# Kernel optimization log

Measured on AMD Instinct MI355X. Metric: run time of the kernel, lower is better.

The kernel has to match this reference:

```python
import jax, jax.numpy as jnp
import numpy as np

N_NODES = 50000
N_EDGES = 800000
D = 128
H = 8
HD = D // H
N_NTYPES = 3
N_ETYPES = 5
LN_EPS = 1e-5


def setup_inputs() -> dict:
    key = jax.random.key(0)
    ks = jax.random.split(key, 16)
    inp = {
        "x": jax.random.normal(ks[0], (N_NODES, D), dtype=jnp.float32),
        "edge_index": jax.random.randint(ks[1], (2, N_EDGES), 0, N_NODES),
        "edge_type": jax.random.randint(ks[2], (N_EDGES,), 0, N_ETYPES),
        "node_type": jax.random.randint(ks[3], (N_NODES,), 0, N_NTYPES),
        # per-(node_type, head) QKV projections, per-(edge_type, head) K transform
        "W_Q": jax.random.normal(ks[4], (N_NTYPES, H, HD, HD), dtype=jnp.float32) * 0.02,
        "W_K": jax.random.normal(ks[5], (N_NTYPES, H, HD, HD), dtype=jnp.float32) * 0.02,
        "W_V": jax.random.normal(ks[6], (N_NTYPES, H, HD, HD), dtype=jnp.float32) * 0.02,
        "W_edge": jax.random.normal(ks[7], (N_ETYPES, H, HD, HD), dtype=jnp.float32) * 0.02,
        "mu": jnp.ones((H, N_ETYPES), dtype=jnp.float32),
        "W_out": jax.random.normal(ks[8], (D, D), dtype=jnp.float32) * 0.02,
        "b_out": jnp.zeros((D,), dtype=jnp.float32),
        "ln1_g": jnp.ones((D,), dtype=jnp.float32),
        "ln1_b": jnp.zeros((D,), dtype=jnp.float32),
        "W1": jax.random.normal(ks[9], (D, 4 * D), dtype=jnp.float32) * 0.02,
        "b1": jnp.zeros((4 * D,), dtype=jnp.float32),
        "W2": jax.random.normal(ks[10], (4 * D, D), dtype=jnp.float32) * 0.02,
        "b2": jnp.zeros((D,), dtype=jnp.float32),
        "ln2_g": jnp.ones((D,), dtype=jnp.float32),
        "ln2_b": jnp.zeros((D,), dtype=jnp.float32),
    }
    return inp


def _layer_norm(y, g, b):
    m = y.mean(-1, keepdims=True)
    v = ((y - m) ** 2).mean(-1, keepdims=True)
    return (y - m) * jax.lax.rsqrt(v + LN_EPS) * g + b


def reference(x, edge_index, edge_type, node_type,
              W_Q, W_K, W_V, W_edge, mu,
              W_out, b_out, ln1_g, ln1_b, W1, b1, W2, b2, ln2_g, ln2_b):
    N = x.shape[0]
    xh = x.reshape(N, H, HD)  # heads vectorized (concat of per-head slices)

    # type-specific QKV: small fixed loop over node types, masked select
    Q = jnp.zeros_like(xh)
    K = jnp.zeros_like(xh)
    V = jnp.zeros_like(xh)
    for t in range(N_NTYPES):
        m = (node_type == t)[:, None, None]
        Q = jnp.where(m, jnp.einsum('nhd,hdf->nhf', xh, W_Q[t]), Q)
        K = jnp.where(m, jnp.einsum('nhd,hdf->nhf', xh, W_K[t]), K)
        V = jnp.where(m, jnp.einsum('nhd,hdf->nhf', xh, W_V[t]), V)

    src, dst = edge_index[0], edge_index[1]
    q_dst = Q[dst]   # [E,H,HD]
    k_src = K[src]   # [E,H,HD]

    # edge-type-specific K transform
    kt = jnp.zeros_like(k_src)
    for et in range(N_ETYPES):
        m = (edge_type == et)[:, None, None]
        kt = jnp.where(m, jnp.einsum('ehd,hdf->ehf', k_src, W_edge[et]), kt)

    scores = (q_dst * kt).sum(-1) / jnp.sqrt(jnp.float32(HD))  # [E,H]
    scores = scores * mu[:, edge_type].T                       # mu per edge type, per head

    # sparse softmax over incoming edges of each dst node, per head
    smax = jax.ops.segment_max(scores, dst, num_segments=N)
    ex = jnp.exp(scores - smax[dst])
    den = jax.ops.segment_sum(ex, dst, num_segments=N)
    w = ex / (den[dst] + 1e-10)                                 # [E,H]

    agg = jax.ops.segment_sum(V[src] * w[..., None], dst, num_segments=N)  # [N,H,HD]
    mh = agg.reshape(N, D) @ W_out + b_out  # dropout is identity in eval

    h = _layer_norm(x + mh, ln1_g, ln1_b)
    ffn = jax.nn.gelu(h @ W1 + b1, approximate=False) @ W2 + b2
    return _layer_norm(h + ffn, ln2_g, ln2_b)
```

## Files before the change

### kernel.cpp

```cpp
#include <hip/hip_runtime.h>
#include <hip/hip_bf16.h>

#define N_NODESC 50000
#define N_EDGESC 800000
#define DD 128
#define HH 8
#define HDIM 16
#define N_NT 3
#define N_ET 5
#define NPB 196
#define NEB 400
#define NFB 512

#define KV8_OFF    ((size_t)0)
#define QT8_OFF    ((size_t)12800000)
#define XP_OFF     ((size_t)44800000)
#define T_OFF      ((size_t)0)
#define AGG_OFF    ((size_t)57600000)
#define H1B_OFF    ((size_t)70400000)
#define WOUTT_OFF  ((size_t)83200000)
#define W1T_OFF    ((size_t)83232768)
#define W2T_OFF    ((size_t)83363840)
#define WALL_OFF   ((size_t)83494912)
#define EDATA_OFF  ((size_t)84183040)
#define ROWS_OFF   ((size_t)87383040)
#define ORIG_OFF   ((size_t)87583104)
#define DEG_OFF    ((size_t)87783104)
#define TOFS_OFF   ((size_t)87983104)
#define BH_OFF     ((size_t)87983168)
#define BB_OFF     ((size_t)87985536)
#define TMP_OFF    ((size_t)87988928)
#define RLOC_OFF   ((size_t)91188928)
#define CSUM_OFF   ((size_t)91389056)

using short8 = __attribute__((ext_vector_type(8))) short;
using f32x4  = __attribute__((ext_vector_type(4))) float;
using f32x2  = __attribute__((ext_vector_type(2))) float;

__device__ __forceinline__ ushort f2b(float f) {
    __hip_bfloat16 h = __float2bfloat16(f);
    return *(ushort*)&h;
}
__device__ __forceinline__ float b2f(ushort u) {
    __hip_bfloat16 h = *(__hip_bfloat16*)&u;
    return __bfloat162float(h);
}
__device__ __forceinline__ f32x2 pk0(unsigned int w) {
    return __builtin_amdgcn_cvt_pk_f32_fp8((int)w, false);
}
__device__ __forceinline__ f32x2 pk1(unsigned int w) {
    return __builtin_amdgcn_cvt_pk_f32_fp8((int)w, true);
}

__global__ __launch_bounds__(256) void prep_a(
    const float* __restrict__ Wout, const float* __restrict__ W1, const float* __restrict__ W2,
    const float* __restrict__ WQ, const float* __restrict__ Wk, const float* __restrict__ Wv,
    const float* __restrict__ We, const float* __restrict__ mu,
    ushort* __restrict__ Woutt, ushort* __restrict__ W1t, ushort* __restrict__ W2t,
    ushort* __restrict__ Wall,
    const int* __restrict__ ntype, int* __restrict__ bh,
    const int* __restrict__ dst, int* __restrict__ deg, unsigned int* __restrict__ tmp)
{
    const int b = blockIdx.x, tid = threadIdx.x;
    if (b < 1920) {
        const int gid = b * 256 + tid;
        if (gid < 16384) {
            const int nn = gid >> 7, k = gid & 127;
            Woutt[gid] = f2b(Wout[k * 128 + nn]);
        } else if (gid < 81920) {
            const int i = gid - 16384;
            const int nn = i >> 7, k = i & 127;
            W1t[i] = f2b(W1[k * 512 + nn]);
        } else if (gid < 147456) {
            const int i = gid - 81920;
            const int nn = i >> 9, k = i & 511;
            W2t[i] = f2b(W2[k * 128 + nn]);
        } else {
            const int idx = gid - 147456;
            const int t = idx / (896 * 128);
            const int rem = idx % (896 * 128);
            const int c = rem / 128, k = rem % 128;
            const int hk = k >> 4, ck = k & 15;
            float v = 0.f;
            if (c < 128) {
                const int hc = c >> 4, j = c & 15;
                if (hk == hc) v = 4.f * Wk[((t * HH + hc) * HDIM + ck) * HDIM + j];
            } else if (c < 256) {
                const int c2 = c - 128, hc = c2 >> 4, j = c2 & 15;
                if (hk == hc) v = 4.f * Wv[((t * HH + hc) * HDIM + ck) * HDIM + j];
            } else {
                const int cq = c - 256, et = cq >> 7, dd = cq & 127;
                const int hq = dd >> 4, j = dd & 15;
                if (hk == hq) {
                    const float* wq = WQ + ((t * HH + hq) * HDIM + ck) * HDIM;
                    const float* we = We + ((et * HH + hq) * HDIM + j) * HDIM;
                    float s = 0.f;
#pragma unroll
                    for (int f = 0; f < 16; f++) s = fmaf(wq[f], we[f], s);
                    v = 64.f * mu[hq * N_ET + et] * s;
                }
            }
            Wall[idx] = f2b(v);
        }
    } else if (b < 1920 + NPB) {
        const int bc = b - 1920;
        const int wave = tid >> 6, lane = tid & 63;
        const int n = bc * 256 + tid;
        const int t = (n < N_NODESC) ? ntype[n] : -1;
        const unsigned long long m0 = __ballot(t == 0);
        const unsigned long long m1 = __ballot(t == 1);
        const unsigned long long m2 = __ballot(t == 2);
        __shared__ int wcnt[4][3];
        if (lane == 0) {
            wcnt[wave][0] = (int)__popcll(m0);
            wcnt[wave][1] = (int)__popcll(m1);
            wcnt[wave][2] = (int)__popcll(m2);
        }
        __syncthreads();
        if (tid < 3)
            bh[tid * NPB + bc] = wcnt[0][tid] + wcnt[1][tid] + wcnt[2][tid] + wcnt[3][tid];
    } else {
        for (int e = (b - 1920 - NPB) * 256 + tid; e < N_EDGESC; e += NEB * 256) {
            const int nd = dst[e];
            const unsigned int p = (unsigned int)atomicAdd(&deg[nd], 1);
            tmp[e] = (p << 16) | (unsigned int)nd;
        }
    }
}

__global__ __launch_bounds__(256) void prep_b(
    const int* __restrict__ bh, const int* __restrict__ deg,
    int* __restrict__ bb, int* __restrict__ tofs,
    int* __restrict__ rloc, int* __restrict__ csum)
{
    __shared__ int part[256];
    const int tid = threadIdx.x;
    if (blockIdx.x == 0) {
        const int base3 = tid * 3;
        int e0 = (base3 + 0 < 588) ? bh[base3 + 0] : 0;
        int e1 = (base3 + 1 < 588) ? bh[base3 + 1] : 0;
        int e2 = (base3 + 2 < 588) ? bh[base3 + 2] : 0;
        const int l0 = e0, l1 = e0 + e1, l2 = l1 + e2;
        part[tid] = l2;
        __syncthreads();
        for (int off = 1; off < 256; off <<= 1) {
            const int u = (tid >= off) ? part[tid - off] : 0;
            __syncthreads();
            part[tid] += u;
            __syncthreads();
        }
        const int tb = part[tid] - l2;
        if (base3 + 0 < 588) bb[base3 + 0] = tb;
        if (base3 + 1 < 588) bb[base3 + 1] = tb + l0;
        if (base3 + 2 < 588) bb[base3 + 2] = tb + l1;
        __syncthreads();
        if (tid == 0) {
            tofs[0] = 0;
            tofs[1] = bb[NPB];
            tofs[2] = bb[2 * NPB];
            tofs[3] = N_NODESC;
        }
    } else {
        const int c = blockIdx.x - 1;
        const int n = c * 256 + tid;
        const int vdeg = (n < N_NODESC) ? deg[n] : 0;
        part[tid] = vdeg;
        __syncthreads();
        for (int off = 1; off < 256; off <<= 1) {
            const int u = (tid >= off) ? part[tid - off] : 0;
            __syncthreads();
            part[tid] += u;
            __syncthreads();
        }
        if (n <= N_NODESC) rloc[n] = part[tid] - vdeg;
        if (tid == 255) csum[c] = part[255];
    }
}

__global__ __launch_bounds__(256) void prep_c(
    const int* __restrict__ ntype, const float* __restrict__ x,
    const int* __restrict__ src, const int* __restrict__ etype,
    const int* __restrict__ bb, const int* __restrict__ rloc, const int* __restrict__ csum,
    const unsigned int* __restrict__ tmp,
    int* __restrict__ origof, ushort* __restrict__ Xp, int* __restrict__ rows,
    int* __restrict__ edata)
{
    const int b = blockIdx.x, tid = threadIdx.x;
    __shared__ int cb[256];
    {
        const int v = (tid < NPB) ? csum[tid] : 0;
        cb[tid] = v;
        __syncthreads();
        for (int off = 1; off < 256; off <<= 1) {
            const int u = (tid >= off) ? cb[tid - off] : 0;
            __syncthreads();
            cb[tid] += u;
            __syncthreads();
        }
        const int incl = cb[tid];
        __syncthreads();
        cb[tid] = incl - v;
        __syncthreads();
    }

    if (b < NPB) {
        const int wave = tid >> 6, lane = tid & 63;
        const int n = b * 256 + tid;
        const int t = (n < N_NODESC) ? ntype[n] : -1;
        const unsigned long long m0 = __ballot(t == 0);
        const unsigned long long m1 = __ballot(t == 1);
        const unsigned long long m2 = __ballot(t == 2);
        __shared__ int wcnt[4][3];
        __shared__ int sp[256];
        if (lane == 0) {
            wcnt[wave][0] = (int)__popcll(m0);
            wcnt[wave][1] = (int)__popcll(m1);
            wcnt[wave][2] = (int)__popcll(m2);
        }
        __syncthreads();
        int p = -1;
        if (n < N_NODESC) {
            int basew = 0;
#pragma unroll
            for (int w = 0; w < 4; w++) if (w < wave) basew += wcnt[w][t];
            const unsigned long long mt = (t == 0) ? m0 : (t == 1) ? m1 : m2;
            const unsigned long long mlt = ((unsigned long long)1 << lane) - 1;
            p = bb[t * NPB + b] + basew + (int)__popcll(mt & mlt);
            origof[p] = n;
        }
        if (n <= N_NODESC) rows[n] = cb[b] + rloc[n];
        sp[tid] = p;
        __syncthreads();
        for (int i = tid; i < 256 * 16; i += 256) {
            const int nn = i >> 4, c = (i & 15) << 3;
            const int pp = sp[nn];
            if (pp < 0) continue;
            const int n2 = b * 256 + nn;
            const float4 v0 = *(const float4*)(x + (size_t)n2 * DD + c);
            const float4 v1 = *(const float4*)(x + (size_t)n2 * DD + c + 4);
            ushort o[8] = {f2b(v0.x), f2b(v0.y), f2b(v0.z), f2b(v0.w),
                           f2b(v1.x), f2b(v1.y), f2b(v1.z), f2b(v1.w)};
            *(uint4*)(Xp + (size_t)pp * DD + c) = *(uint4*)o;
        }
    } else {
        for (int e = (b - NPB) * 256 + tid; e < N_EDGESC; e += NFB * 256) {
            const unsigned int v = tmp[e];
            const int nd = (int)(v & 0xffffu);
            const int p = (int)(v >> 16);
            edata[cb[nd >> 8] + rloc[nd] + p] = src[e] | (etype[e] << 16);
        }
    }
}

#define LDP 40

__global__ __launch_bounds__(256) void proj_gemm(
    const ushort* __restrict__ Xp, const ushort* __restrict__ Wall,
    const int* __restrict__ tofs, const int* __restrict__ origof,
    ushort* __restrict__ KV8, unsigned char* __restrict__ Qt8)
{
    const int t = blockIdx.z;
    const int rs = tofs[t], re = tofs[t + 1];
    const int mBase = rs + blockIdx.x * 128;
    if (mBase >= re) return;
    const int nBase = blockIdx.y * 128;
    const ushort* Bt = Wall + (size_t)t * 896 * 128;

    __shared__ ushort As[128 * LDP];
    __shared__ ushort Bs[128 * LDP];
    const int tid = threadIdx.x;
    const int lane = tid & 63, wave = tid >> 6;
    const int mw = (wave >> 1) * 64, nw = (wave & 1) * 64;
    const int l15 = lane & 15, q8 = (lane >> 4) * 8;

    f32x4 acc[4][4];
#pragma unroll
    for (int i = 0; i < 4; i++)
#pragma unroll
        for (int j = 0; j < 4; j++) acc[i][j] = (f32x4){0.f, 0.f, 0.f, 0.f};

    const int r0 = tid >> 2, c0 = (tid & 3) * 8;
    int rA0 = mBase + r0;      if (rA0 >= N_NODESC) rA0 = N_NODESC - 1;
    int rA1 = mBase + r0 + 64; if (rA1 >= N_NODESC) rA1 = N_NODESC - 1;

    for (int kk = 0; kk < 128; kk += 32) {
        short8 a0 = *(const short8*)(Xp + (size_t)rA0 * DD + kk + c0);
        short8 a1 = *(const short8*)(Xp + (size_t)rA1 * DD + kk + c0);
        short8 b0 = *(const short8*)(Bt + (size_t)(nBase + r0) * 128 + kk + c0);
        short8 b1 = *(const short8*)(Bt + (size_t)(nBase + r0 + 64) * 128 + kk + c0);
        *(short8*)&As[r0 * LDP + c0] = a0;
        *(short8*)&As[(r0 + 64) * LDP + c0] = a1;
        *(short8*)&Bs[r0 * LDP + c0] = b0;
        *(short8*)&Bs[(r0 + 64) * LDP + c0] = b1;
        __syncthreads();
        short8 af[4], bf[4];
#pragma unroll
        for (int i = 0; i < 4; i++)
            af[i] = *(const short8*)&As[(mw + i * 16 + l15) * LDP + q8];
#pragma unroll
        for (int j = 0; j < 4; j++)
            bf[j] = *(const short8*)&Bs[(nw + j * 16 + l15) * LDP + q8];
#pragma unroll
        for (int i = 0; i < 4; i++)
#pragma unroll
            for (int j = 0; j < 4; j++)
                acc[i][j] = __builtin_amdgcn_mfma_f32_16x16x32_bf16(af[i], bf[j], acc[i][j], 0, 0, 0);
        __syncthreads();
    }

    unsigned char* kvb = (unsigned char*)KV8;
    const int rq = (lane >> 4) * 4;
#pragma unroll
    for (int i = 0; i < 4; i++) {
#pragma unroll
        for (int r = 0; r < 4; r++) {
            const int gm = mBase + mw + i * 16 + rq + r;
            if (gm >= re) continue;
            const int og = origof[gm];
#pragma unroll
            for (int j = 0; j < 4; j++) {
                const int gn = nBase + nw + j * 16 + l15;
                const float v = acc[i][j][r];
                const unsigned char b8 =
                    (unsigned char)(__builtin_amdgcn_cvt_pk_fp8_f32(v, v, 0, false) & 0xff);
                if (gn < 256) kvb[(size_t)og * 256 + gn] = b8;
                else          Qt8[(size_t)og * 640 + (gn - 256)] = b8;
            }
        }
    }
}

__global__ __launch_bounds__(128) void edgeagg_kernel(
    const int* __restrict__ rowstart, const int* __restrict__ edata,
    const unsigned char* __restrict__ Qt8, const unsigned char* __restrict__ KV8,
    ushort* __restrict__ agg)
{
    const int w = threadIdx.x >> 6;
    const int lane = threadIdx.x & 63;
    const int n = blockIdx.x * 2 + w;
    const int slot = lane >> 3;
    const int h = lane & 7;

    __shared__ uint4 qs8s[2][40];
    if (lane < 40)
        qs8s[w][lane] = ((const uint4*)(Qt8 + (size_t)n * 640))[lane];
    __syncthreads();
    const uint* qbase = (const uint*)&qs8s[w][0];

    const int s0 = rowstart[n], s1 = rowstart[n + 1];
    const float qsc = 1.44269504f / 1024.f;

    float acc[16];
#pragma unroll
    for (int j = 0; j < 16; j++) acc[j] = 0.f;
    float den = 0.f;

    for (int i = s0 + slot; i < s1; i += 8) {
        const int ed = edata[i];
        const int sn = ed & 0xffff;
        const int et = ed >> 16;
        const unsigned char* kvp = KV8 + ((size_t)sn << 8);
        const uint4 kw = *(const uint4*)(kvp + (h << 4));
        const uint4 vw = *(const uint4*)(kvp + 128 + (h << 4));
        const uint4 qw = *(const uint4*)(qbase + (et << 5) + (h << 2));

        const f32x2 q0 = pk0(qw.x), q1 = pk1(qw.x), q2 = pk0(qw.y), q3 = pk1(qw.y);
        const f32x2 q4 = pk0(qw.z), q5 = pk1(qw.z), q6 = pk0(qw.w), q7 = pk1(qw.w);
        const f32x2 k0 = pk0(kw.x), k1 = pk1(kw.x), k2 = pk0(kw.y), k3 = pk1(kw.y);
        const f32x2 k4 = pk0(kw.z), k5 = pk1(kw.z), k6 = pk0(kw.w), k7 = pk1(kw.w);

        float pa = q0.x * k0.x;
        float pb = q0.y * k0.y;
        float pc = q1.x * k1.x;
        float pd = q1.y * k1.y;
        pa = fmaf(q2.x, k2.x, pa); pb = fmaf(q2.y, k2.y, pb);
        pc = fmaf(q3.x, k3.x, pc); pd = fmaf(q3.y, k3.y, pd);
        pa = fmaf(q4.x, k4.x, pa); pb = fmaf(q4.y, k4.y, pb);
        pc = fmaf(q5.x, k5.x, pc); pd = fmaf(q5.y, k5.y, pd);
        pa = fmaf(q6.x, k6.x, pa); pb = fmaf(q6.y, k6.y, pb);
        pc = fmaf(q7.x, k7.x, pc); pd = fmaf(q7.y, k7.y, pd);

        const float ex = exp2f(((pa + pb) + (pc + pd)) * qsc);
        den += ex;

        const f32x2 v0 = pk0(vw.x), v1 = pk1(vw.x), v2 = pk0(vw.y), v3 = pk1(vw.y);
        const f32x2 v4 = pk0(vw.z), v5 = pk1(vw.z), v6 = pk0(vw.w), v7 = pk1(vw.w);
        acc[0]  = fmaf(ex, v0.x, acc[0]);  acc[1]  = fmaf(ex, v0.y, acc[1]);
        acc[2]  = fmaf(ex, v1.x, acc[2]);  acc[3]  = fmaf(ex, v1.y, acc[3]);
        acc[4]  = fmaf(ex, v2.x, acc[4]);  acc[5]  = fmaf(ex, v2.y, acc[5]);
        acc[6]  = fmaf(ex, v3.x, acc[6]);  acc[7]  = fmaf(ex, v3.y, acc[7]);
        acc[8]  = fmaf(ex, v4.x, acc[8]);  acc[9]  = fmaf(ex, v4.y, acc[9]);
        acc[10] = fmaf(ex, v5.x, acc[10]); acc[11] = fmaf(ex, v5.y, acc[11]);
        acc[12] = fmaf(ex, v6.x, acc[12]); acc[13] = fmaf(ex, v6.y, acc[13]);
        acc[14] = fmaf(ex, v7.x, acc[14]); acc[15] = fmaf(ex, v7.y, acc[15]);
    }

    {
        const int b0 = slot & 1, b1 = slot & 2, b2 = slot & 4;
#pragma unroll
        for (int j = 0; j < 8; j++) {
            const float v = b0 ? acc[j] : acc[j + 8];
            const float r = __shfl_xor(v, 8);
            acc[j] = (b0 ? acc[j + 8] : acc[j]) + r;
        }
#pragma unroll
        for (int j = 0; j < 4; j++) {
            const float v = b1 ? acc[j] : acc[j + 4];
            const float r = __shfl_xor(v, 16);
            acc[j] = (b1 ? acc[j + 4] : acc[j]) + r;
        }
#pragma unroll
        for (int j = 0; j < 2; j++) {
            const float v = b2 ? acc[j] : acc[j + 2];
            const float r = __shfl_xor(v, 32);
            acc[j] = (b2 ? acc[j + 2] : acc[j]) + r;
        }
        den += __shfl_xor(den, 8);
        den += __shfl_xor(den, 16);
        den += __shfl_xor(den, 32);
    }
    const float rr = 0.25f / (den + 1e-10f);
    const int fb = (h << 4) + ((slot & 1) << 3) + ((slot & 2) << 1) + ((slot & 4) >> 1);
    ushort o2[2] = { f2b(acc[0] * rr), f2b(acc[1] * rr) };
    *(uint*)&agg[((size_t)n << 7) + fb] = *(uint*)o2;
}

template<int KT, int EPI>
__global__ __launch_bounds__(256) void mfma_gemm(
    const ushort* __restrict__ A, const ushort* __restrict__ Bt,
    const float* __restrict__ bias,
    const float* __restrict__ residF, const ushort* __restrict__ residB,
    const float* __restrict__ g, const float* __restrict__ b,
    float* __restrict__ outF, ushort* __restrict__ outB, int ldOut)
{
    __shared__ ushort As[128 * LDP];
    __shared__ ushort Bs[128 * LDP];
    __shared__ float red[2][2][128];
    const int tid = threadIdx.x;
    const int lane = tid & 63, wave = tid >> 6;
    const int mw = (wave >> 1) * 64, nw = (wave & 1) * 64;
    const int mBase = blockIdx.x * 128, nBase = blockIdx.y * 128;
    const int l15 = lane & 15, q8 = (lane >> 4) * 8;

    f32x4 acc[4][4];
#pragma unroll
    for (int i = 0; i < 4; i++)
#pragma unroll
        for (int j = 0; j < 4; j++) acc[i][j] = (f32x4){0.f, 0.f, 0.f, 0.f};

    const int r0 = tid >> 2;
    const int c0 = (tid & 3) * 8;

    for (int kk = 0; kk < KT; kk += 32) {
        const ushort* pa = A  + (size_t)(mBase + r0) * KT + kk + c0;
        const ushort* pb = Bt + (size_t)(nBase + r0) * KT + kk + c0;
        short8 a0 = *(const short8*)pa;
        short8 a1 = *(const short8*)(pa + (size_t)64 * KT);
        short8 b0 = *(const short8*)pb;
        short8 b1 = *(const short8*)(pb + (size_t)64 * KT);
        *(short8*)&As[r0 * LDP + c0] = a0;
        *(short8*)&As[(r0 + 64) * LDP + c0] = a1;
        *(short8*)&Bs[r0 * LDP + c0] = b0;
        *(short8*)&Bs[(r0 + 64) * LDP + c0] = b1;
        __syncthreads();

        short8 af[4], bf[4];
#pragma unroll
        for (int i = 0; i < 4; i++)
            af[i] = *(const short8*)&As[(mw + i * 16 + l15) * LDP + q8];
#pragma unroll
        for (int j = 0; j < 4; j++)
            bf[j] = *(const short8*)&Bs[(nw + j * 16 + l15) * LDP + q8];
#pragma unroll
        for (int i = 0; i < 4; i++)
#pragma unroll
            for (int j = 0; j < 4; j++)
                acc[i][j] = __builtin_amdgcn_mfma_f32_16x16x32_bf16(af[i], bf[j], acc[i][j], 0, 0, 0);
        __syncthreads();
    }

    const int rq = (lane >> 4) * 4;

    if (EPI == 0) {
#pragma unroll
        for (int i = 0; i < 4; i++) {
#pragma unroll
            for (int r = 0; r < 4; r++) {
                const int gm = mBase + mw + i * 16 + rq + r;
                if (gm >= N_NODESC) continue;
#pragma unroll
                for (int j = 0; j < 4; j++) {
                    const int gn = nBase + nw + j * 16 + l15;
                    float v = acc[i][j][r] + bias[gn];
                    v = 0.5f * v * (1.f + erff(v * 0.70710678118654752f));
                    outB[(size_t)gm * ldOut + gn] = f2b(v);
                }
            }
        }
    } else {
        float biasv[4], gv[4], bv[4];
#pragma unroll
        for (int j = 0; j < 4; j++) {
            const int gn = nw + j * 16 + l15;
            biasv[j] = bias[gn]; gv[j] = g[gn]; bv[j] = b[gn];
        }
#pragma unroll
        for (int i = 0; i < 4; i++) {
#pragma unroll
            for (int r = 0; r < 4; r++) {
                const int row = mw + i * 16 + rq + r;
                const int gm = mBase + row;
                float s = 0.f, ss = 0.f;
#pragma unroll
                for (int j = 0; j < 4; j++) {
                    const int gn = nw + j * 16 + l15;
                    float v = acc[i][j][r] + biasv[j];
                    if (EPI == 1) v += (gm < N_NODESC) ? residF[(size_t)gm * DD + gn] : 0.f;
                    else          v += (gm < N_NODESC) ? b2f(residB[(size_t)gm * DD + gn]) : 0.f;
                    acc[i][j][r] = v;
                    s += v; ss += v * v;
                }
                s  += __shfl_xor(s, 1);  s  += __shfl_xor(s, 2);  s  += __shfl_xor(s, 4);  s  += __shfl_xor(s, 8);
                ss += __shfl_xor(ss, 1); ss += __shfl_xor(ss, 2); ss += __shfl_xor(ss, 4); ss += __shfl_xor(ss, 8);
                if (l15 == 0) { red[0][nw >> 6][row] = s; red[1][nw >> 6][row] = ss; }
            }
        }
        __syncthreads();
#pragma unroll
        for (int i = 0; i < 4; i++) {
#pragma unroll
            for (int r = 0; r < 4; r++) {
                const int row = mw + i * 16 + rq + r;
                const int gm = mBase + row;
                if (gm >= N_NODESC) continue;
                const float s  = red[0][0][row] + red[0][1][row];
                const float ss = red[1][0][row] + red[1][1][row];
                const float mean = s * (1.f / 128.f);
                const float var  = ss * (1.f / 128.f) - mean * mean;
                const float rstd = rsqrtf(var + 1e-5f);
#pragma unroll
                for (int j = 0; j < 4; j++) {
                    const int gn = nw + j * 16 + l15;
                    const float o = (acc[i][j][r] - mean) * rstd * gv[j] + bv[j];
                    if (EPI == 1) outB[(size_t)gm * DD + gn] = f2b(o);
                    else          outF[(size_t)gm * DD + gn] = o;
                }
            }
        }
    }
}

extern "C" void kernel_launch(void* const* d_in, const int* in_sizes, int n_in,
                              void* d_out, int out_size, void* d_ws, size_t ws_size,
                              hipStream_t stream)
{
    const float* x     = (const float*)d_in[0];
    const int*   ei    = (const int*)d_in[1];
    const int*   etyp  = (const int*)d_in[2];
    const int*   ntype = (const int*)d_in[3];
    const float* Wq    = (const float*)d_in[4];
    const float* Wk    = (const float*)d_in[5];
    const float* Wv    = (const float*)d_in[6];
    const float* We    = (const float*)d_in[7];
    const float* mu    = (const float*)d_in[8];
    const float* Wout  = (const float*)d_in[9];
    const float* bout  = (const float*)d_in[10];
    const float* g1    = (const float*)d_in[11];
    const float* b1ln  = (const float*)d_in[12];
    const float* W1    = (const float*)d_in[13];
    const float* b1    = (const float*)d_in[14];
    const float* W2    = (const float*)d_in[15];
    const float* b2    = (const float*)d_in[16];
    const float* g2    = (const float*)d_in[17];
    const float* b2ln  = (const float*)d_in[18];
    float* out = (float*)d_out;

    char* ws = (char*)d_ws;
    ushort*        KV8   = (ushort*)(ws + KV8_OFF);
    unsigned char* Qt8   = (unsigned char*)(ws + QT8_OFF);
    ushort*        Xp    = (ushort*)(ws + XP_OFF);
    ushort*        T     = (ushort*)(ws + T_OFF);
    ushort*        agg   = (ushort*)(ws + AGG_OFF);
    ushort*        h1b   = (ushort*)(ws + H1B_OFF);
    ushort*        Woutt = (ushort*)(ws + WOUTT_OFF);
    ushort*        W1t   = (ushort*)(ws + W1T_OFF);
    ushort*        W2t   = (ushort*)(ws + W2T_OFF);
    ushort*        Wall  = (ushort*)(ws + WALL_OFF);
    int*           edata = (int*)(ws + EDATA_OFF);
    int*           rows  = (int*)(ws + ROWS_OFF);
    int*           origof= (int*)(ws + ORIG_OFF);
    int*           deg   = (int*)(ws + DEG_OFF);
    int*           tofs  = (int*)(ws + TOFS_OFF);
    int*           bh    = (int*)(ws + BH_OFF);
    int*           bb    = (int*)(ws + BB_OFF);
    unsigned int*  tmp   = (unsigned int*)(ws + TMP_OFF);
    int*           rloc  = (int*)(ws + RLOC_OFF);
    int*           csum  = (int*)(ws + CSUM_OFF);

    const int* srcA = ei;
    const int* dstA = ei + N_EDGESC;

    (void)hipMemsetAsync(ws + DEG_OFF, 0, 200000, stream);

    prep_a<<<1920 + NPB + NEB, 256, 0, stream>>>(
        Wout, W1, W2, Wq, Wk, Wv, We, mu, Woutt, W1t, W2t, Wall,
        ntype, bh, dstA, deg, tmp);
    prep_b<<<1 + NPB, 256, 0, stream>>>(bh, deg, bb, tofs, rloc, csum);
    prep_c<<<NPB + NFB, 256, 0, stream>>>(ntype, x, srcA, etyp, bb, rloc, csum, tmp,
                                          origof, Xp, rows, edata);

    proj_gemm<<<dim3(394, 7, 3), 256, 0, stream>>>(Xp, Wall, tofs, origof, KV8, Qt8);
    edgeagg_kernel<<<N_NODESC / 2, 128, 0, stream>>>(rows, edata, Qt8,
                                                     (const unsigned char*)KV8, agg);

    mfma_gemm<128, 1><<<391, 256, 0, stream>>>(agg, Woutt, bout, x, nullptr, g1, b1ln, nullptr, h1b, 128);
    mfma_gemm<128, 0><<<dim3(391, 4), 256, 0, stream>>>(h1b, W1t, b1, nullptr, nullptr, nullptr, nullptr, nullptr, T, 512);
    mfma_gemm<512, 2><<<391, 256, 0, stream>>>(T, W2t, b2, nullptr, h1b, g2, b2ln, out, nullptr, 128);
}
```

Before: 356.3 us.

## Fuse output projection, LayerNorms and FFN into one tail kernel

Replaces the three separate MFMA GEMM launches (out-proj+LN1, W1+GELU, W2+LN2) with a single kernel on 64-row tiles. The LN1 output stays in shared memory, and the 512-wide hidden activation is produced and consumed in 128-column chunks without touching global memory. This removes the round trips of h1b and the large T intermediate through HBM plus two launches. In exchange it uses smaller M tiles with more syncs and weight reloads per block, and it also changes the LDS padding LDP from 40 to 36, which affects proj_gemm too.

```diff
diff --git a/kernel.cpp b/kernel.cpp
--- a/kernel.cpp
+++ b/kernel.cpp
@@ -15,9 +15,7 @@
 #define KV8_OFF    ((size_t)0)
 #define QT8_OFF    ((size_t)12800000)
 #define XP_OFF     ((size_t)44800000)
-#define T_OFF      ((size_t)0)
 #define AGG_OFF    ((size_t)57600000)
-#define H1B_OFF    ((size_t)70400000)
 #define WOUTT_OFF  ((size_t)83200000)
 #define W1T_OFF    ((size_t)83232768)
 #define W2T_OFF    ((size_t)83363840)
@@ -50,6 +48,9 @@
 }
 __device__ __forceinline__ f32x2 pk1(unsigned int w) {
     return __builtin_amdgcn_cvt_pk_f32_fp8((int)w, true);
+}
+__device__ __forceinline__ float gelu_f(float v) {
+    return 0.5f * v * (1.f + erff(v * 0.70710678118654752f));
 }
 
 __global__ __launch_bounds__(256) void prep_a(
@@ -252,7 +253,7 @@
     }
 }
 
-#define LDP 40
+#define LDP 36
 
 __global__ __launch_bounds__(256) void proj_gemm(
     const ushort* __restrict__ Xp, const ushort* __restrict__ Wall,
@@ -425,112 +426,210 @@
     *(uint*)&agg[((size_t)n << 7) + fb] = *(uint*)o2;
 }
 
-template<int KT, int EPI>
-__global__ __launch_bounds__(256) void mfma_gemm(
-    const ushort* __restrict__ A, const ushort* __restrict__ Bt,
-    const float* __restrict__ bias,
-    const float* __restrict__ residF, const ushort* __restrict__ residB,
-    const float* __restrict__ g, const float* __restrict__ b,
-    float* __restrict__ outF, ushort* __restrict__ outB, int ldOut)
+#define LDH 132
+
+__global__ __launch_bounds__(256) void fused_tail(
+    const ushort* __restrict__ agg, const ushort* __restrict__ Woutt,
+    const ushort* __restrict__ W1t, const ushort* __restrict__ W2t,
+    const float* __restrict__ x,
+    const float* __restrict__ bout, const float* __restrict__ g1, const float* __restrict__ b1ln,
+    const float* __restrict__ b1, const float* __restrict__ b2,
+    const float* __restrict__ g2, const float* __restrict__ b2ln,
+    float* __restrict__ out)
 {
-    __shared__ ushort As[128 * LDP];
+    __shared__ ushort Hs[64 * LDH];
+    __shared__ ushort As[64 * LDP];
     __shared__ ushort Bs[128 * LDP];
-    __shared__ float red[2][2][128];
+    __shared__ float red[2][2][64];
+
     const int tid = threadIdx.x;
     const int lane = tid & 63, wave = tid >> 6;
-    const int mw = (wave >> 1) * 64, nw = (wave & 1) * 64;
-    const int mBase = blockIdx.x * 128, nBase = blockIdx.y * 128;
-    const int l15 = lane & 15, q8 = (lane >> 4) * 8;
-
-    f32x4 acc[4][4];
-#pragma unroll
-    for (int i = 0; i < 4; i++)
-#pragma unroll
-        for (int j = 0; j < 4; j++) acc[i][j] = (f32x4){0.f, 0.f, 0.f, 0.f};
-
-    const int r0 = tid >> 2;
-    const int c0 = (tid & 3) * 8;
-
-    for (int kk = 0; kk < KT; kk += 32) {
-        const ushort* pa = A  + (size_t)(mBase + r0) * KT + kk + c0;
-        const ushort* pb = Bt + (size_t)(nBase + r0) * KT + kk + c0;
-        short8 a0 = *(const short8*)pa;
-        short8 a1 = *(const short8*)(pa + (size_t)64 * KT);
-        short8 b0 = *(const short8*)pb;
-        short8 b1 = *(const short8*)(pb + (size_t)64 * KT);
-        *(short8*)&As[r0 * LDP + c0] = a0;
-        *(short8*)&As[(r0 + 64) * LDP + c0] = a1;
-        *(short8*)&Bs[r0 * LDP + c0] = b0;
-        *(short8*)&Bs[(r0 + 64) * LDP + c0] = b1;
-        __syncthreads();
-
-        short8 af[4], bf[4];
-#pragma unroll
-        for (int i = 0; i < 4; i++)
-            af[i] = *(const short8*)&As[(mw + i * 16 + l15) * LDP + q8];
+    const int wm = wave >> 1, wn = wave & 1;
+    const int l15 = lane & 15, q8 = (lane >> 4) * 8, rq = (lane >> 4) * 4;
+    const int mBase = blockIdx.x * 64;
+
+    const int rA = tid >> 2, c0 = (tid & 3) * 8;
+    int rowA = mBase + rA; if (rowA >= N_NODESC) rowA = N_NODESC - 1;
+
+    f32x4 acc1[2][4], acc2[2][4];
+#pragma unroll
+    for (int i = 0; i < 2; i++)
+#pragma unroll
+        for (int j = 0; j < 4; j++) {
+            acc1[i][j] = (f32x4){0.f, 0.f, 0.f, 0.f};
+            acc2[i][j] = (f32x4){0.f, 0.f, 0.f, 0.f};
+        }
+
+    for (int kk = 0; kk < 128; kk += 32) {
+        short8 a0 = *(const short8*)(agg + (size_t)rowA * DD + kk + c0);
+        short8 b0 = *(const short8*)(Woutt + (size_t)rA * 128 + kk + c0);
+        short8 b1r = *(const short8*)(Woutt + (size_t)(rA + 64) * 128 + kk + c0);
+        *(short8*)&As[rA * LDP + c0] = a0;
+        *(short8*)&Bs[rA * LDP + c0] = b0;
+        *(short8*)&Bs[(rA + 64) * LDP + c0] = b1r;
+        __syncthreads();
+        short8 af[2], bf[4];
+#pragma unroll
+        for (int i = 0; i < 2; i++)
+            af[i] = *(const short8*)&As[(wm * 32 + i * 16 + l15) * LDP + q8];
 #pragma unroll
         for (int j = 0; j < 4; j++)
-            bf[j] = *(const short8*)&Bs[(nw + j * 16 + l15) * LDP + q8];
-#pragma unroll
-        for (int i = 0; i < 4; i++)
+            bf[j] = *(const short8*)&Bs[(wn * 64 + j * 16 + l15) * LDP + q8];
+#pragma unroll
+        for (int i = 0; i < 2; i++)
 #pragma unroll
             for (int j = 0; j < 4; j++)
-                acc[i][j] = __builtin_amdgcn_mfma_f32_16x16x32_bf16(af[i], bf[j], acc[i][j], 0, 0, 0);
-        __syncthreads();
-    }
-
-    const int rq = (lane >> 4) * 4;
-
-    if (EPI == 0) {
-#pragma unroll
-        for (int i = 0; i < 4; i++) {
+                acc1[i][j] = __builtin_amdgcn_mfma_f32_16x16x32_bf16(af[i], bf[j], acc1[i][j], 0, 0, 0);
+        __syncthreads();
+    }
+
+    {
+        float boutv[4], gv[4], bv[4];
+#pragma unroll
+        for (int j = 0; j < 4; j++) {
+            const int gn = wn * 64 + j * 16 + l15;
+            boutv[j] = bout[gn]; gv[j] = g1[gn]; bv[j] = b1ln[gn];
+        }
+#pragma unroll
+        for (int i = 0; i < 2; i++) {
 #pragma unroll
             for (int r = 0; r < 4; r++) {
-                const int gm = mBase + mw + i * 16 + rq + r;
-                if (gm >= N_NODESC) continue;
-#pragma unroll
-                for (int j = 0; j < 4; j++) {
-                    const int gn = nBase + nw + j * 16 + l15;
-                    float v = acc[i][j][r] + bias[gn];
-                    v = 0.5f * v * (1.f + erff(v * 0.70710678118654752f));
-                    outB[(size_t)gm * ldOut + gn] = f2b(v);
-                }
-            }
-        }
-    } else {
-        float biasv[4], gv[4], bv[4];
-#pragma unroll
-        for (int j = 0; j < 4; j++) {
-            const int gn = nw + j * 16 + l15;
-            biasv[j] = bias[gn]; gv[j] = g[gn]; bv[j] = b[gn];
-        }
-#pragma unroll
-        for (int i = 0; i < 4; i++) {
-#pragma unroll
-            for (int r = 0; r < 4; r++) {
-                const int row = mw + i * 16 + rq + r;
+                const int row = wm * 32 + i * 16 + rq + r;
                 const int gm = mBase + row;
                 float s = 0.f, ss = 0.f;
 #pragma unroll
                 for (int j = 0; j < 4; j++) {
-                    const int gn = nw + j * 16 + l15;
-                    float v = acc[i][j][r] + biasv[j];
-                    if (EPI == 1) v += (gm < N_NODESC) ? residF[(size_t)gm * DD + gn] : 0.f;
-                    else          v += (gm < N_NODESC) ? b2f(residB[(size_t)gm * DD + gn]) : 0.f;
-                    acc[i][j][r] = v;
+                    const int gn = wn * 64 + j * 16 + l15;
+                    float v = acc1[i][j][r] + boutv[j];
+                    v += (gm < N_NODESC) ? x[(size_t)gm * DD + gn] : 0.f;
+                    acc1[i][j][r] = v;
                     s += v; ss += v * v;
                 }
                 s  += __shfl_xor(s, 1);  s  += __shfl_xor(s, 2);  s  += __shfl_xor(s, 4);  s  += __shfl_xor(s, 8);
                 ss += __shfl_xor(ss, 1); ss += __shfl_xor(ss, 2); ss += __shfl_xor(ss, 4); ss += __shfl_xor(ss, 8);
-                if (l15 == 0) { red[0][nw >> 6][row] = s; red[1][nw >> 6][row] = ss; }
+                if (l15 == 0) { red[0][wn][row] = s; red[1][wn][row] = ss; }
             }
         }
         __syncthreads();
 #pragma unroll
-        for (int i = 0; i < 4; i++) {
+        for (int i = 0; i < 2; i++) {
 #pragma unroll
             for (int r = 0; r < 4; r++) {
-                const int row = mw + i * 16 + rq + r;
+                const int row = wm * 32 + i * 16 + rq + r;
+                const float s  = red[0][0][row] + red[0][1][row];
+                const float ss = red[1][0][row] + red[1][1][row];
+                const float mean = s * (1.f / 128.f);
+                const float var  = ss * (1.f / 128.f) - mean * mean;
+                const float rstd = rsqrtf(var + 1e-5f);
+#pragma unroll
+                for (int j = 0; j < 4; j++) {
+                    const int gn = wn * 64 + j * 16 + l15;
+                    const float o = (acc1[i][j][r] - mean) * rstd * gv[j] + bv[j];
+                    Hs[row * LDH + gn] = f2b(o);
+                }
+            }
+        }
+        __syncthreads();
+    }
+
+    for (int nb = 0; nb < 4; nb++) {
+#pragma unroll
+        for (int i = 0; i < 2; i++)
+#pragma unroll
+            for (int j = 0; j < 4; j++) acc1[i][j] = (f32x4){0.f, 0.f, 0.f, 0.f};
+
+        for (int kk = 0; kk < 128; kk += 32) {
+            short8 b0 = *(const short8*)(W1t + (size_t)(nb * 128 + rA) * 128 + kk + c0);
+            short8 b1r = *(const short8*)(W1t + (size_t)(nb * 128 + rA + 64) * 128 + kk + c0);
+            *(short8*)&Bs[rA * LDP + c0] = b0;
+            *(short8*)&Bs[(rA + 64) * LDP + c0] = b1r;
+            __syncthreads();
+            short8 af[2], bf[4];
+#pragma unroll
+            for (int i = 0; i < 2; i++)
+                af[i] = *(const short8*)&Hs[(wm * 32 + i * 16 + l15) * LDH + kk + q8];
+#pragma unroll
+            for (int j = 0; j < 4; j++)
+                bf[j] = *(const short8*)&Bs[(wn * 64 + j * 16 + l15) * LDP + q8];
+#pragma unroll
+            for (int i = 0; i < 2; i++)
+#pragma unroll
+                for (int j = 0; j < 4; j++)
+                    acc1[i][j] = __builtin_amdgcn_mfma_f32_16x16x32_bf16(af[i], bf[j], acc1[i][j], 0, 0, 0);
+            __syncthreads();
+        }
+
+        float b1v[4];
+#pragma unroll
+        for (int j = 0; j < 4; j++)
+            b1v[j] = b1[nb * 128 + wn * 64 + j * 16 + l15];
+
+        for (int kk2 = 0; kk2 < 4; kk2++) {
+            short8 b0 = *(const short8*)(W2t + (size_t)rA * 512 + nb * 128 + kk2 * 32 + c0);
+            short8 b1r = *(const short8*)(W2t + (size_t)(rA + 64) * 512 + nb * 128 + kk2 * 32 + c0);
+            *(short8*)&Bs[rA * LDP + c0] = b0;
+            *(short8*)&Bs[(rA + 64) * LDP + c0] = b1r;
+            if (wn == (kk2 >> 1)) {
+                const int j0 = 2 * (kk2 & 1);
+#pragma unroll
+                for (int i = 0; i < 2; i++)
+#pragma unroll
+                    for (int jj = 0; jj < 2; jj++)
+#pragma unroll
+                        for (int r = 0; r < 4; r++) {
+                            const int row = wm * 32 + i * 16 + rq + r;
+                            const float v = gelu_f(acc1[i][j0 + jj][r] + b1v[j0 + jj]);
+                            As[row * LDP + jj * 16 + l15] = f2b(v);
+                        }
+            }
+            __syncthreads();
+            short8 af[2], bf[4];
+#pragma unroll
+            for (int i = 0; i < 2; i++)
+                af[i] = *(const short8*)&As[(wm * 32 + i * 16 + l15) * LDP + q8];
+#pragma unroll
+            for (int j = 0; j < 4; j++)
+                bf[j] = *(const short8*)&Bs[(wn * 64 + j * 16 + l15) * LDP + q8];
+#pragma unroll
+            for (int i = 0; i < 2; i++)
+#pragma unroll
+                for (int j = 0; j < 4; j++)
+                    acc2[i][j] = __builtin_amdgcn_mfma_f32_16x16x32_bf16(af[i], bf[j], acc2[i][j], 0, 0, 0);
+            __syncthreads();
+        }
+    }
+
+    {
+        float b2v[4], gv[4], bv[4];
+#pragma unroll
+        for (int j = 0; j < 4; j++) {
+            const int gn = wn * 64 + j * 16 + l15;
+            b2v[j] = b2[gn]; gv[j] = g2[gn]; bv[j] = b2ln[gn];
+        }
+#pragma unroll
+        for (int i = 0; i < 2; i++) {
+#pragma unroll
+            for (int r = 0; r < 4; r++) {
+                const int row = wm * 32 + i * 16 + rq + r;
+                float s = 0.f, ss = 0.f;
+#pragma unroll
+                for (int j = 0; j < 4; j++) {
+                    const int gn = wn * 64 + j * 16 + l15;
+                    float v = acc2[i][j][r] + b2v[j] + b2f(Hs[row * LDH + gn]);
+                    acc2[i][j][r] = v;
+                    s += v; ss += v * v;
+                }
+                s  += __shfl_xor(s, 1);  s  += __shfl_xor(s, 2);  s  += __shfl_xor(s, 4);  s  += __shfl_xor(s, 8);
+                ss += __shfl_xor(ss, 1); ss += __shfl_xor(ss, 2); ss += __shfl_xor(ss, 4); ss += __shfl_xor(ss, 8);
+                if (l15 == 0) { red[0][wn][row] = s; red[1][wn][row] = ss; }
+            }
+        }
+        __syncthreads();
+#pragma unroll
+        for (int i = 0; i < 2; i++) {
+#pragma unroll
+            for (int r = 0; r < 4; r++) {
+                const int row = wm * 32 + i * 16 + rq + r;
                 const int gm = mBase + row;
                 if (gm >= N_NODESC) continue;
                 const float s  = red[0][0][row] + red[0][1][row];
@@ -540,10 +639,8 @@
                 const float rstd = rsqrtf(var + 1e-5f);
 #pragma unroll
                 for (int j = 0; j < 4; j++) {
-                    const int gn = nw + j * 16 + l15;
-                    const float o = (acc[i][j][r] - mean) * rstd * gv[j] + bv[j];
-                    if (EPI == 1) outB[(size_t)gm * DD + gn] = f2b(o);
-                    else          outF[(size_t)gm * DD + gn] = o;
+                    const int gn = wn * 64 + j * 16 + l15;
+                    out[(size_t)gm * DD + gn] = (acc2[i][j][r] - mean) * rstd * gv[j] + bv[j];
                 }
             }
         }
@@ -579,9 +676,7 @@
     ushort*        KV8   = (ushort*)(ws + KV8_OFF);
     unsigned char* Qt8   = (unsigned char*)(ws + QT8_OFF);
     ushort*        Xp    = (ushort*)(ws + XP_OFF);
-    ushort*        T     = (ushort*)(ws + T_OFF);
     ushort*        agg   = (ushort*)(ws + AGG_OFF);
-    ushort*        h1b   = (ushort*)(ws + H1B_OFF);
     ushort*        Woutt = (ushort*)(ws + WOUTT_OFF);
     ushort*        W1t   = (ushort*)(ws + W1T_OFF);
     ushort*        W2t   = (ushort*)(ws + W2T_OFF);
@@ -613,7 +708,6 @@
     edgeagg_kernel<<<N_NODESC / 2, 128, 0, stream>>>(rows, edata, Qt8,
                                                      (const unsigned char*)KV8, agg);
 
-    mfma_gemm<128, 1><<<391, 256, 0, stream>>>(agg, Woutt, bout, x, nullptr, g1, b1ln, nullptr, h1b, 128);
-    mfma_gemm<128, 0><<<dim3(391, 4), 256, 0, stream>>>(h1b, W1t, b1, nullptr, nullptr, nullptr, nullptr, nullptr, T, 512);
-    mfma_gemm<512, 2><<<391, 256, 0, stream>>>(T, W2t, b2, nullptr, h1b, g2, b2ln, out, nullptr, 128);
-}
+    fused_tail<<<782, 256, 0, stream>>>(agg, Woutt, W1t, W2t, x,
+                                        bout, g1, b1ln, b1, b2, g2, b2ln, out);
+}
```

New measurement: 342.4 us. 3.9% less time.

## Fuse output projection, LayerNorms and FFN into one per-row-tile tail kernel

Applied to the files above, without the earlier changes.

Replaces the three separate GEMM launches (W_out+LN1, W1+GELU, W2+LN2) with one kernel. Each wave owns 16 rows and runs the full tail, keeping the h1 and GELU intermediates in shared memory instead of writing the 512-wide intermediate to global. Weight fragments are read directly from global (L2) with no shared staging, and there is no inter-wave reduction. This removes intermediate HBM traffic and launch overhead, but adds redundant weight reads and less data reuse per block. The shared-memory padding for proj_gemm also changes from 40 to 36.

```diff
diff --git a/kernel.cpp b/kernel.cpp
--- a/kernel.cpp
+++ b/kernel.cpp
@@ -15,9 +15,7 @@
 #define KV8_OFF    ((size_t)0)
 #define QT8_OFF    ((size_t)12800000)
 #define XP_OFF     ((size_t)44800000)
-#define T_OFF      ((size_t)0)
 #define AGG_OFF    ((size_t)57600000)
-#define H1B_OFF    ((size_t)70400000)
 #define WOUTT_OFF  ((size_t)83200000)
 #define W1T_OFF    ((size_t)83232768)
 #define W2T_OFF    ((size_t)83363840)
@@ -50,6 +48,9 @@
 }
 __device__ __forceinline__ f32x2 pk1(unsigned int w) {
     return __builtin_amdgcn_cvt_pk_f32_fp8((int)w, true);
+}
+__device__ __forceinline__ float gelu_f(float v) {
+    return 0.5f * v * (1.f + erff(v * 0.70710678118654752f));
 }
 
 __global__ __launch_bounds__(256) void prep_a(
@@ -252,7 +253,7 @@
     }
 }
 
-#define LDP 40
+#define LDP 36
 
 __global__ __launch_bounds__(256) void proj_gemm(
     const ushort* __restrict__ Xp, const ushort* __restrict__ Wall,
@@ -425,126 +426,128 @@
     *(uint*)&agg[((size_t)n << 7) + fb] = *(uint*)o2;
 }
 
-template<int KT, int EPI>
-__global__ __launch_bounds__(256) void mfma_gemm(
-    const ushort* __restrict__ A, const ushort* __restrict__ Bt,
-    const float* __restrict__ bias,
-    const float* __restrict__ residF, const ushort* __restrict__ residB,
-    const float* __restrict__ g, const float* __restrict__ b,
-    float* __restrict__ outF, ushort* __restrict__ outB, int ldOut)
+#define LDH 132
+
+__global__ __launch_bounds__(256) void fused_tail(
+    const ushort* __restrict__ agg, const ushort* __restrict__ Woutt,
+    const ushort* __restrict__ W1t, const ushort* __restrict__ W2t,
+    const float* __restrict__ x,
+    const float* __restrict__ bout, const float* __restrict__ g1, const float* __restrict__ b1ln,
+    const float* __restrict__ b1, const float* __restrict__ b2,
+    const float* __restrict__ g2, const float* __restrict__ b2ln,
+    float* __restrict__ out)
 {
-    __shared__ ushort As[128 * LDP];
-    __shared__ ushort Bs[128 * LDP];
-    __shared__ float red[2][2][128];
+    __shared__ ushort Hs[64 * LDH];
+    __shared__ ushort Ts[64 * LDH];
+
     const int tid = threadIdx.x;
-    const int lane = tid & 63, wave = tid >> 6;
-    const int mw = (wave >> 1) * 64, nw = (wave & 1) * 64;
-    const int mBase = blockIdx.x * 128, nBase = blockIdx.y * 128;
-    const int l15 = lane & 15, q8 = (lane >> 4) * 8;
-
-    f32x4 acc[4][4];
-#pragma unroll
-    for (int i = 0; i < 4; i++)
-#pragma unroll
-        for (int j = 0; j < 4; j++) acc[i][j] = (f32x4){0.f, 0.f, 0.f, 0.f};
-
-    const int r0 = tid >> 2;
-    const int c0 = (tid & 3) * 8;
-
-    for (int kk = 0; kk < KT; kk += 32) {
-        const ushort* pa = A  + (size_t)(mBase + r0) * KT + kk + c0;
-        const ushort* pb = Bt + (size_t)(nBase + r0) * KT + kk + c0;
-        short8 a0 = *(const short8*)pa;
-        short8 a1 = *(const short8*)(pa + (size_t)64 * KT);
-        short8 b0 = *(const short8*)pb;
-        short8 b1 = *(const short8*)(pb + (size_t)64 * KT);
-        *(short8*)&As[r0 * LDP + c0] = a0;
-        *(short8*)&As[(r0 + 64) * LDP + c0] = a1;
-        *(short8*)&Bs[r0 * LDP + c0] = b0;
-        *(short8*)&Bs[(r0 + 64) * LDP + c0] = b1;
-        __syncthreads();
-
-        short8 af[4], bf[4];
-#pragma unroll
-        for (int i = 0; i < 4; i++)
-            af[i] = *(const short8*)&As[(mw + i * 16 + l15) * LDP + q8];
-#pragma unroll
-        for (int j = 0; j < 4; j++)
-            bf[j] = *(const short8*)&Bs[(nw + j * 16 + l15) * LDP + q8];
-#pragma unroll
-        for (int i = 0; i < 4; i++)
-#pragma unroll
-            for (int j = 0; j < 4; j++)
-                acc[i][j] = __builtin_amdgcn_mfma_f32_16x16x32_bf16(af[i], bf[j], acc[i][j], 0, 0, 0);
-        __syncthreads();
-    }
-
-    const int rq = (lane >> 4) * 4;
-
-    if (EPI == 0) {
-#pragma unroll
-        for (int i = 0; i < 4; i++) {
-#pragma unroll
-            for (int r = 0; r < 4; r++) {
-                const int gm = mBase + mw + i * 16 + rq + r;
-                if (gm >= N_NODESC) continue;
-#pragma unroll
-                for (int j = 0; j < 4; j++) {
-                    const int gn = nBase + nw + j * 16 + l15;
-                    float v = acc[i][j][r] + bias[gn];
-                    v = 0.5f * v * (1.f + erff(v * 0.70710678118654752f));
-                    outB[(size_t)gm * ldOut + gn] = f2b(v);
-                }
+    const int lane = tid & 63, wv = tid >> 6;
+    const int l15 = lane & 15, q8 = (lane >> 4) * 8, rq = (lane >> 4) * 4;
+    const int rbase = blockIdx.x * 64 + wv * 16;
+    const int lbase = wv * 16;
+
+    int arow = rbase + l15;
+    if (arow >= N_NODESC) arow = N_NODESC - 1;
+
+    f32x4 acc1[8], acc2[8];
+#pragma unroll
+    for (int j = 0; j < 8; j++) {
+        acc1[j] = (f32x4){0.f, 0.f, 0.f, 0.f};
+        acc2[j] = (f32x4){0.f, 0.f, 0.f, 0.f};
+    }
+
+#pragma unroll
+    for (int kk = 0; kk < 4; kk++) {
+        const short8 af = *(const short8*)(agg + (size_t)arow * DD + kk * 32 + q8);
+#pragma unroll
+        for (int j = 0; j < 8; j++) {
+            const short8 bf = *(const short8*)(Woutt + (size_t)(j * 16 + l15) * 128 + kk * 32 + q8);
+            acc1[j] = __builtin_amdgcn_mfma_f32_16x16x32_bf16(af, bf, acc1[j], 0, 0, 0);
+        }
+    }
+
+#pragma unroll
+    for (int r = 0; r < 4; r++) {
+        const int grow = rbase + rq + r;
+        const int gr = (grow < N_NODESC) ? grow : N_NODESC - 1;
+        const int lrow = lbase + rq + r;
+        float v[8];
+        float s = 0.f, ss = 0.f;
+#pragma unroll
+        for (int j = 0; j < 8; j++) {
+            const int col = j * 16 + l15;
+            const float t = acc1[j][r] + bout[col] + x[(size_t)gr * DD + col];
+            v[j] = t; s += t; ss += t * t;
+        }
+        s  += __shfl_xor(s, 1);  s  += __shfl_xor(s, 2);  s  += __shfl_xor(s, 4);  s  += __shfl_xor(s, 8);
+        ss += __shfl_xor(ss, 1); ss += __shfl_xor(ss, 2); ss += __shfl_xor(ss, 4); ss += __shfl_xor(ss, 8);
+        const float mean = s * (1.f / 128.f);
+        const float var  = ss * (1.f / 128.f) - mean * mean;
+        const float rstd = rsqrtf(var + 1e-5f);
+#pragma unroll
+        for (int j = 0; j < 8; j++) {
+            const int col = j * 16 + l15;
+            Hs[lrow * LDH + col] = f2b((v[j] - mean) * rstd * g1[col] + b1ln[col]);
+        }
+    }
+
+    for (int nb = 0; nb < 4; nb++) {
+        f32x4 a1[8];
+#pragma unroll
+        for (int j = 0; j < 8; j++) a1[j] = (f32x4){0.f, 0.f, 0.f, 0.f};
+
+#pragma unroll
+        for (int kk = 0; kk < 4; kk++) {
+            const short8 af = *(const short8*)&Hs[(lbase + l15) * LDH + kk * 32 + q8];
+#pragma unroll
+            for (int j = 0; j < 8; j++) {
+                const short8 bf = *(const short8*)(W1t + (size_t)(nb * 128 + j * 16 + l15) * 128 + kk * 32 + q8);
+                a1[j] = __builtin_amdgcn_mfma_f32_16x16x32_bf16(af, bf, a1[j], 0, 0, 0);
             }
         }
-    } else {
-        float biasv[4], gv[4], bv[4];
-#pragma unroll
-        for (int j = 0; j < 4; j++) {
-            const int gn = nw + j * 16 + l15;
-            biasv[j] = bias[gn]; gv[j] = g[gn]; bv[j] = b[gn];
-        }
-#pragma unroll
-        for (int i = 0; i < 4; i++) {
-#pragma unroll
-            for (int r = 0; r < 4; r++) {
-                const int row = mw + i * 16 + rq + r;
-                const int gm = mBase + row;
-                float s = 0.f, ss = 0.f;
-#pragma unroll
-                for (int j = 0; j < 4; j++) {
-                    const int gn = nw + j * 16 + l15;
-                    float v = acc[i][j][r] + biasv[j];
-                    if (EPI == 1) v += (gm < N_NODESC) ? residF[(size_t)gm * DD + gn] : 0.f;
-                    else          v += (gm < N_NODESC) ? b2f(residB[(size_t)gm * DD + gn]) : 0.f;
-                    acc[i][j][r] = v;
-                    s += v; ss += v * v;
-                }
-                s  += __shfl_xor(s, 1);  s  += __shfl_xor(s, 2);  s  += __shfl_xor(s, 4);  s  += __shfl_xor(s, 8);
-                ss += __shfl_xor(ss, 1); ss += __shfl_xor(ss, 2); ss += __shfl_xor(ss, 4); ss += __shfl_xor(ss, 8);
-                if (l15 == 0) { red[0][nw >> 6][row] = s; red[1][nw >> 6][row] = ss; }
+
+#pragma unroll
+        for (int j = 0; j < 8; j++) {
+            const int col = j * 16 + l15;
+            const float bb = b1[nb * 128 + col];
+#pragma unroll
+            for (int r = 0; r < 4; r++)
+                Ts[(lbase + rq + r) * LDH + col] = f2b(gelu_f(a1[j][r] + bb));
+        }
+
+#pragma unroll
+        for (int kk = 0; kk < 4; kk++) {
+            const short8 af = *(const short8*)&Ts[(lbase + l15) * LDH + kk * 32 + q8];
+#pragma unroll
+            for (int j = 0; j < 8; j++) {
+                const short8 bf = *(const short8*)(W2t + (size_t)(j * 16 + l15) * 512 + nb * 128 + kk * 32 + q8);
+                acc2[j] = __builtin_amdgcn_mfma_f32_16x16x32_bf16(af, bf, acc2[j], 0, 0, 0);
             }
         }
-        __syncthreads();
-#pragma unroll
-        for (int i = 0; i < 4; i++) {
-#pragma unroll
-            for (int r = 0; r < 4; r++) {
-                const int row = mw + i * 16 + rq + r;
-                const int gm = mBase + row;
-                if (gm >= N_NODESC) continue;
-                const float s  = red[0][0][row] + red[0][1][row];
-                const float ss = red[1][0][row] + red[1][1][row];
-                const float mean = s * (1.f / 128.f);
-                const float var  = ss * (1.f / 128.f) - mean * mean;
-                const float rstd = rsqrtf(var + 1e-5f);
-#pragma unroll
-                for (int j = 0; j < 4; j++) {
-                    const int gn = nw + j * 16 + l15;
-                    const float o = (acc[i][j][r] - mean) * rstd * gv[j] + bv[j];
-                    if (EPI == 1) outB[(size_t)gm * DD + gn] = f2b(o);
-                    else          outF[(size_t)gm * DD + gn] = o;
-                }
+    }
+
+#pragma unroll
+    for (int r = 0; r < 4; r++) {
+        const int grow = rbase + rq + r;
+        const int lrow = lbase + rq + r;
+        float v[8];
+        float s = 0.f, ss = 0.f;
+#pragma unroll
+        for (int j = 0; j < 8; j++) {
+            const int col = j * 16 + l15;
+            const float t = acc2[j][r] + b2[col] + b2f(Hs[lrow * LDH + col]);
+            v[j] = t; s += t; ss += t * t;
+        }
+        s  += __shfl_xor(s, 1);  s  += __shfl_xor(s, 2);  s  += __shfl_xor(s, 4);  s  += __shfl_xor(s, 8);
+        ss += __shfl_xor(ss, 1); ss += __shfl_xor(ss, 2); ss += __shfl_xor(ss, 4); ss += __shfl_xor(ss, 8);
+        const float mean = s * (1.f / 128.f);
+        const float var  = ss * (1.f / 128.f) - mean * mean;
+        const float rstd = rsqrtf(var + 1e-5f);
+        if (grow < N_NODESC) {
+#pragma unroll
+            for (int j = 0; j < 8; j++) {
+                const int col = j * 16 + l15;
+                out[(size_t)grow * DD + col] = (v[j] - mean) * rstd * g2[col] + b2ln[col];
             }
         }
     }
@@ -579,9 +582,7 @@
     ushort*        KV8   = (ushort*)(ws + KV8_OFF);
     unsigned char* Qt8   = (unsigned char*)(ws + QT8_OFF);
     ushort*        Xp    = (ushort*)(ws + XP_OFF);
-    ushort*        T     = (ushort*)(ws + T_OFF);
     ushort*        agg   = (ushort*)(ws + AGG_OFF);
-    ushort*        h1b   = (ushort*)(ws + H1B_OFF);
     ushort*        Woutt = (ushort*)(ws + WOUTT_OFF);
     ushort*        W1t   = (ushort*)(ws + W1T_OFF);
     ushort*        W2t   = (ushort*)(ws + W2T_OFF);
@@ -613,7 +614,6 @@
     edgeagg_kernel<<<N_NODESC / 2, 128, 0, stream>>>(rows, edata, Qt8,
                                                      (const unsigned char*)KV8, agg);
 
-    mfma_gemm<128, 1><<<391, 256, 0, stream>>>(agg, Woutt, bout, x, nullptr, g1, b1ln, nullptr, h1b, 128);
-    mfma_gemm<128, 0><<<dim3(391, 4), 256, 0, stream>>>(h1b, W1t, b1, nullptr, nullptr, nullptr, nullptr, nullptr, T, 512);
-    mfma_gemm<512, 2><<<391, 256, 0, stream>>>(T, W2t, b2, nullptr, h1b, g2, b2ln, out, nullptr, 128);
-}
+    fused_tail<<<782, 256, 0, stream>>>(agg, Woutt, W1t, W2t, x,
+                                        bout, g1, b1ln, b1, b2, g2, b2ln, out);
+}
```

New measurement: 418.5 us. 1.17x slower.
